# Optimization experiments

Measured on AMD Instinct MI355X. Metric: run time of the kernel, lower is better.

The kernel has to match this reference:

```python
import jax, jax.numpy as jnp
import numpy as np

NUM_LSTMS = 2
INPUT_DIM = 1
HIDDEN_DIM = 32
OUTPUT_DIM = 1


def _init_cell(key, in_dim, hid):
    k1, k2, k3, k4 = jax.random.split(key, 4)
    s = 1.0 / np.sqrt(hid)
    Wih = jax.random.uniform(k1, (4 * hid, in_dim), minval=-s, maxval=s, dtype=jnp.float32)
    Whh = jax.random.uniform(k2, (4 * hid, hid), minval=-s, maxval=s, dtype=jnp.float32)
    bih = jax.random.uniform(k3, (4 * hid,), minval=-s, maxval=s, dtype=jnp.float32)
    bhh = jax.random.uniform(k4, (4 * hid,), minval=-s, maxval=s, dtype=jnp.float32)
    # forget-gate bias (second quarter in PyTorch i,f,g,o layout) filled with 1.0
    bih = bih.at[hid:2 * hid].set(1.0)
    bhh = bhh.at[hid:2 * hid].set(1.0)
    return Wih, Whh, bih, bhh


def setup_inputs() -> dict:
    key = jax.random.key(0)
    kx, k0, k1, kl = jax.random.split(key, 4)
    B, T = 2048, 1024
    x = jax.random.normal(kx, (B, T), dtype=jnp.float32)
    Wih0, Whh0, bih0, bhh0 = _init_cell(k0, INPUT_DIM, HIDDEN_DIM)
    Wih1, Whh1, bih1, bhh1 = _init_cell(k1, HIDDEN_DIM, HIDDEN_DIM)
    kw, kb = jax.random.split(kl)
    s = 1.0 / np.sqrt(HIDDEN_DIM)
    Wlin = jax.random.uniform(kw, (OUTPUT_DIM, HIDDEN_DIM), minval=-s, maxval=s, dtype=jnp.float32)
    blin = jax.random.uniform(kb, (OUTPUT_DIM,), minval=-s, maxval=s, dtype=jnp.float32)
    return {"x": x, "Wih0": Wih0, "Whh0": Whh0, "bih0": bih0, "bhh0": bhh0,
            "Wih1": Wih1, "Whh1": Whh1, "bih1": bih1, "bhh1": bhh1,
            "Wlin": Wlin, "blin": blin}


def _lstm_cell(x_t, h, c, Wih, Whh, bih, bhh):
    # PyTorch LSTMCell gate layout: i, f, g, o
    g = x_t @ Wih.T + bih + h @ Whh.T + bhh  # [B, 4H]
    i, f, gg, o = jnp.split(g, 4, axis=-1)
    i = jax.nn.sigmoid(i)
    f = jax.nn.sigmoid(f)
    gg = jnp.tanh(gg)
    o = jax.nn.sigmoid(o)
    c_new = f * c + i * gg
    h_new = o * jnp.tanh(c_new)
    return h_new, c_new


def reference(x, Wih0, Whh0, bih0, bhh0, Wih1, Whh1, bih1, bhh1, Wlin, blin):
    B, T = x.shape
    params = [(Wih0, Whh0, bih0, bhh0), (Wih1, Whh1, bih1, bhh1)]
    h0 = [jnp.zeros((B, HIDDEN_DIM), jnp.float32) for _ in range(NUM_LSTMS)]
    c0 = [jnp.zeros((B, HIDDEN_DIM), jnp.float32) for _ in range(NUM_LSTMS)]

    xs = x.T[:, :, None]  # [T, B, 1]

    def step(carry, x_t):
        hs, cs = carry
        hs, cs = list(hs), list(cs)
        inp = x_t
        for j in range(NUM_LSTMS):
            hs[j], cs[j] = _lstm_cell(inp, hs[j], cs[j], *params[j])
            inp = hs[j]
        out = hs[-1] @ Wlin.T + blin  # [B, 1]
        return (tuple(hs), tuple(cs)), out

    _, outs = jax.lax.scan(step, (tuple(h0), tuple(c0)), xs)  # [T, B, 1]
    return outs[:, :, 0].T  # [B, T]
```

## Files before the change

kernel.cpp:

```cpp
#include <hip/hip_runtime.h>


typedef _Float16 h2 __attribute__((ext_vector_type(2)));
typedef _Float16 h8 __attribute__((ext_vector_type(8)));

constexpr int BATCH = 2048;
constexpr int TLEN  = 1024;
constexpr int HID   = 32;
constexpr float L2E = 1.44269504088896f;

union H8U { h8 v; h2 p[4]; };

static __device__ __forceinline__ float rcp_f(float v){ return __builtin_amdgcn_rcpf(v); }
static __device__ __forceinline__ float exp2_f(float v){ return __builtin_amdgcn_exp2f(v); }
static __device__ __forceinline__ float bcastf(float v, int k){
    return __int_as_float(__builtin_amdgcn_readlane(__float_as_int(v), k));
}
static __device__ __forceinline__ float dot2(h2 a, h2 b, float c){
    return __builtin_amdgcn_fdot2(a, b, c, false);
}
static __device__ __forceinline__ int pki(float a, float b){
    h2 r; r.x = (_Float16)a; r.y = (_Float16)b;
    return __builtin_bit_cast(int, r);
}
static __device__ __forceinline__ h2 asp(int v){ return __builtin_bit_cast(h2, v); }
static __device__ __forceinline__ float xchg32(float v, int xaddr){
    return __int_as_float(__builtin_amdgcn_ds_bpermute(xaddr, __float_as_int(v)));
}

__global__ void __launch_bounds__(256) __attribute__((amdgpu_waves_per_eu(2, 2)))
lstm2_v9(const float* __restrict__ x,
         const float* __restrict__ Wih0, const float* __restrict__ Whh0,
         const float* __restrict__ bih0, const float* __restrict__ bhh0,
         const float* __restrict__ Wih1, const float* __restrict__ Whh1,
         const float* __restrict__ bih1, const float* __restrict__ bhh1,
         const float* __restrict__ Wlin, const float* __restrict__ blin,
         float* __restrict__ out)
{
    const int tid  = threadIdx.x;
    const int lane = tid & 63;
    const int w    = tid >> 6;
    const int b    = blockIdx.x * 4 + w;
    const int j    = lane & 31;
    const int hi   = lane >> 5;
    const int rowA = hi * 64 + j;
    const int rowB = rowA + 32;
    const int xaddr = (lane ^ 32) << 2;

    __shared__ alignas(16) _Float16 hb0s[4][32];
    __shared__ alignas(16) _Float16 hstore[4][64][40];
    __shared__ alignas(16) _Float16 wls[4][32];

    _Float16* hb0p = &hb0s[w][0];

    wls[w][j] = (_Float16)Wlin[j];

    int wA0i[16], wB0i[16], iA1i[16], iB1i[16], hA1i[16], hB1i[16];
    #pragma unroll
    for (int m = 0; m < 16; ++m){
        wA0i[m] = pki(Whh0[rowA * HID + 2*m], Whh0[rowA * HID + 2*m + 1]);
        wB0i[m] = pki(Whh0[rowB * HID + 2*m], Whh0[rowB * HID + 2*m + 1]);
        iA1i[m] = pki(Wih1[rowA * HID + 2*m], Wih1[rowA * HID + 2*m + 1]);
        iB1i[m] = pki(Wih1[rowB * HID + 2*m], Wih1[rowB * HID + 2*m + 1]);
        hA1i[m] = pki(Whh1[rowA * HID + 2*m], Whh1[rowA * HID + 2*m + 1]);
        hB1i[m] = pki(Whh1[rowB * HID + 2*m], Whh1[rowB * HID + 2*m + 1]);
    }
    #pragma unroll
    for (int m = 0; m < 16; ++m){
        asm volatile("" : "+v"(wA0i[m]), "+v"(wB0i[m]), "+v"(iA1i[m]),
                          "+v"(iB1i[m]), "+v"(hA1i[m]), "+v"(hB1i[m]));
    }

    float wa0 = Wih0[rowA];
    float wb0 = Wih0[rowB];
    float ba0 = bih0[rowA] + bhh0[rowA];
    float bb0 = bih0[rowB] + bhh0[rowB];
    float ba1 = bih1[rowA] + bhh1[rowA];
    float bb1 = bih1[rowB] + bhh1[rowB];
    float bl  = blin[0];
    asm volatile("" : "+v"(wa0), "+v"(wb0), "+v"(ba0), "+v"(bb0),
                      "+v"(ba1), "+v"(bb1), "+v"(bl));

    const float kA = hi ? (-2.0f * L2E) : (-L2E);
    const float mA = hi ?  2.0f : 1.0f;
    const float cA = hi ? -1.0f : 0.0f;

    float c0 = 0.0f, c1 = 0.0f;
    H8U hp0[4], hp1[4];
    #pragma unroll
    for (int m = 0; m < 4; ++m){
        hp0[m].v = (h8)(_Float16)0.0f;
        hp1[m].v = (h8)(_Float16)0.0f;
    }

    const float* xrow = x   + (size_t)b * TLEN;
    float*       orow = out + (size_t)b * TLEN;

    for (int tc = 0; tc < TLEN / 64; ++tc){
        const float xchunk = xrow[tc * 64 + lane];

        for (int tt = 0; tt < 64; ++tt){
            const float xt = bcastf(xchunk, tt);

            float ga  = __builtin_fmaf(wa0, xt, ba0);
            float gb  = __builtin_fmaf(wb0, xt, bb0);
            float ga2 = 0.0f, gb2 = 0.0f;
            #pragma unroll
            for (int m = 0; m < 4; ++m){
                ga  = dot2(asp(wA0i[4*m+0]), hp0[m].p[0], ga );
                gb  = dot2(asp(wB0i[4*m+0]), hp0[m].p[0], gb );
                ga2 = dot2(asp(wA0i[4*m+1]), hp0[m].p[1], ga2);
                gb2 = dot2(asp(wB0i[4*m+1]), hp0[m].p[1], gb2);
                ga  = dot2(asp(wA0i[4*m+2]), hp0[m].p[2], ga );
                gb  = dot2(asp(wB0i[4*m+2]), hp0[m].p[2], gb );
                ga2 = dot2(asp(wA0i[4*m+3]), hp0[m].p[3], ga2);
                gb2 = dot2(asp(wB0i[4*m+3]), hp0[m].p[3], gb2);
            }
            ga += ga2; gb += gb2;

            float act_a = __builtin_fmaf(mA, rcp_f(1.0f + exp2_f(ga * kA)), cA);
            float act_b = rcp_f(1.0f + exp2_f(gb * (-L2E)));
            const float oa = xchg32(act_a, xaddr);
            const float ob = xchg32(act_b, xaddr);
            {
                const float fsel = hi ? ob : act_b;
                const float osel = hi ? act_b : ob;
                c0 = __builtin_fmaf(fsel, c0, act_a * oa);
                const float t0 = __builtin_fmaf(2.0f,
                        rcp_f(1.0f + exp2_f(c0 * (-2.0f * L2E))), -1.0f);
                const float h0 = osel * t0;
                hb0p[j] = (_Float16)h0;
            }
            {
                const h8* hv = (const h8*)hb0p;
                #pragma unroll
                for (int m = 0; m < 4; ++m) hp0[m].v = hv[m];
            }

            float pa = ba1, pb = bb1, pa2 = 0.0f, pb2 = 0.0f;
            float qa = 0.0f, qb = 0.0f, qa2 = 0.0f, qb2 = 0.0f;
            #pragma unroll
            for (int m = 0; m < 4; ++m){
                pa  = dot2(asp(iA1i[4*m+0]), hp0[m].p[0], pa );
                pb  = dot2(asp(iB1i[4*m+0]), hp0[m].p[0], pb );
                qa  = dot2(asp(hA1i[4*m+0]), hp1[m].p[0], qa );
                qb  = dot2(asp(hB1i[4*m+0]), hp1[m].p[0], qb );
                pa2 = dot2(asp(iA1i[4*m+1]), hp0[m].p[1], pa2);
                pb2 = dot2(asp(iB1i[4*m+1]), hp0[m].p[1], pb2);
                qa2 = dot2(asp(hA1i[4*m+1]), hp1[m].p[1], qa2);
                qb2 = dot2(asp(hB1i[4*m+1]), hp1[m].p[1], qb2);
                pa  = dot2(asp(iA1i[4*m+2]), hp0[m].p[2], pa );
                pb  = dot2(asp(iB1i[4*m+2]), hp0[m].p[2], pb );
                qa  = dot2(asp(hA1i[4*m+2]), hp1[m].p[2], qa );
                qb  = dot2(asp(hB1i[4*m+2]), hp1[m].p[2], qb );
                pa2 = dot2(asp(iA1i[4*m+3]), hp0[m].p[3], pa2);
                pb2 = dot2(asp(iB1i[4*m+3]), hp0[m].p[3], pb2);
                qa2 = dot2(asp(hA1i[4*m+3]), hp1[m].p[3], qa2);
                qb2 = dot2(asp(hB1i[4*m+3]), hp1[m].p[3], qb2);
            }
            const float g1a = (pa + pa2) + (qa + qa2);
            const float g1b = (pb + pb2) + (qb + qb2);

            float act_a1 = __builtin_fmaf(mA, rcp_f(1.0f + exp2_f(g1a * kA)), cA);
            float act_b1 = rcp_f(1.0f + exp2_f(g1b * (-L2E)));
            const float oa1 = xchg32(act_a1, xaddr);
            const float ob1 = xchg32(act_b1, xaddr);
            {
                const float fsel = hi ? ob1 : act_b1;
                const float osel = hi ? act_b1 : ob1;
                c1 = __builtin_fmaf(fsel, c1, act_a1 * oa1);
                const float t1 = __builtin_fmaf(2.0f,
                        rcp_f(1.0f + exp2_f(c1 * (-2.0f * L2E))), -1.0f);
                const float h1 = osel * t1;
                hstore[w][tt][j] = (_Float16)h1;
            }
            {
                const h8* hv = (const h8*)&hstore[w][tt][0];
                #pragma unroll
                for (int m = 0; m < 4; ++m) hp1[m].v = hv[m];
            }
        }

        {
            H8U wl4[4], hr[4];
            const h8* wv = (const h8*)&wls[w][0];
            const h8* hv = (const h8*)&hstore[w][lane][0];
            #pragma unroll
            for (int m = 0; m < 4; ++m){ wl4[m].v = wv[m]; hr[m].v = hv[m]; }
            float y = bl, y2 = 0.0f;
            #pragma unroll
            for (int m = 0; m < 4; ++m){
                y  = dot2(wl4[m].p[0], hr[m].p[0], y );
                y2 = dot2(wl4[m].p[1], hr[m].p[1], y2);
                y  = dot2(wl4[m].p[2], hr[m].p[2], y );
                y2 = dot2(wl4[m].p[3], hr[m].p[3], y2);
            }
            orow[tc * 64 + lane] = y + y2;
        }
    }
}

extern "C" void kernel_launch(void* const* d_in, const int* in_sizes, int n_in,
                              void* d_out, int out_size, void* d_ws, size_t ws_size,
                              hipStream_t stream) {
    const float* x    = (const float*)d_in[0];
    const float* Wih0 = (const float*)d_in[1];
    const float* Whh0 = (const float*)d_in[2];
    const float* bih0 = (const float*)d_in[3];
    const float* bhh0 = (const float*)d_in[4];
    const float* Wih1 = (const float*)d_in[5];
    const float* Whh1 = (const float*)d_in[6];
    const float* bih1 = (const float*)d_in[7];
    const float* bhh1 = (const float*)d_in[8];
    const float* Wlin = (const float*)d_in[9];
    const float* blin = (const float*)d_in[10];
    float* outp = (float*)d_out;

    dim3 block(256);
    dim3 grid(BATCH / 4);
    hipLaunchKernelGGL(lstm2_v9, grid, block, 0, stream,
                       x, Wih0, Whh0, bih0, bhh0, Wih1, Whh1, bih1, bhh1,
                       Wlin, blin, outp);
}
```

Before: 713.5 us.

## Split LSTM layers across producer/consumer waves with a double-buffered ring

Each batch row now has two waves: one runs layer 0 and one runs layer 1, lagging by a step. Layer-0 hidden states pass through a two-slot shared-memory ring, with a block-wide barrier every timestep. The goal is to run the two layers' recurrences concurrently, shortening the serial dependency chain per step and halving per-wave weight registers. The cost is a __syncthreads every step across 8 waves and twice the waves per batch row, which could cut occupancy headroom or add barrier stalls.

Measured after the change: 1.043 ms. 46.2% more time.

```diff
diff --git a/kernel.cpp b/kernel.cpp
--- a/kernel.cpp
+++ b/kernel.cpp
@@ -28,79 +28,58 @@
     return __int_as_float(__builtin_amdgcn_ds_bpermute(xaddr, __float_as_int(v)));
 }
 
-__global__ void __launch_bounds__(256) __attribute__((amdgpu_waves_per_eu(2, 2)))
-lstm2_v9(const float* __restrict__ x,
-         const float* __restrict__ Wih0, const float* __restrict__ Whh0,
-         const float* __restrict__ bih0, const float* __restrict__ bhh0,
-         const float* __restrict__ Wih1, const float* __restrict__ Whh1,
-         const float* __restrict__ bih1, const float* __restrict__ bhh1,
-         const float* __restrict__ Wlin, const float* __restrict__ blin,
-         float* __restrict__ out)
+__global__ void __launch_bounds__(512)
+lstm2_v11(const float* __restrict__ x,
+          const float* __restrict__ Wih0, const float* __restrict__ Whh0,
+          const float* __restrict__ bih0, const float* __restrict__ bhh0,
+          const float* __restrict__ Wih1, const float* __restrict__ Whh1,
+          const float* __restrict__ bih1, const float* __restrict__ bhh1,
+          const float* __restrict__ Wlin, const float* __restrict__ blin,
+          float* __restrict__ out)
 {
     const int tid  = threadIdx.x;
     const int lane = tid & 63;
-    const int w    = tid >> 6;
-    const int b    = blockIdx.x * 4 + w;
+    const int wid  = tid >> 6;
+    const int role = wid >> 2;
+    const int rw   = wid & 3;
+    const int b    = blockIdx.x * 4 + rw;
     const int j    = lane & 31;
     const int hi   = lane >> 5;
     const int rowA = hi * 64 + j;
     const int rowB = rowA + 32;
     const int xaddr = (lane ^ 32) << 2;
 
-    __shared__ alignas(16) _Float16 hb0s[4][32];
+    __shared__ alignas(16) _Float16 ring[2][4][32];
     __shared__ alignas(16) _Float16 hstore[4][64][40];
-    __shared__ alignas(16) _Float16 wls[4][32];
-
-    _Float16* hb0p = &hb0s[w][0];
-
-    wls[w][j] = (_Float16)Wlin[j];
-
-    int wA0i[16], wB0i[16], iA1i[16], iB1i[16], hA1i[16], hB1i[16];
-    #pragma unroll
-    for (int m = 0; m < 16; ++m){
-        wA0i[m] = pki(Whh0[rowA * HID + 2*m], Whh0[rowA * HID + 2*m + 1]);
-        wB0i[m] = pki(Whh0[rowB * HID + 2*m], Whh0[rowB * HID + 2*m + 1]);
-        iA1i[m] = pki(Wih1[rowA * HID + 2*m], Wih1[rowA * HID + 2*m + 1]);
-        iB1i[m] = pki(Wih1[rowB * HID + 2*m], Wih1[rowB * HID + 2*m + 1]);
-        hA1i[m] = pki(Whh1[rowA * HID + 2*m], Whh1[rowA * HID + 2*m + 1]);
-        hB1i[m] = pki(Whh1[rowB * HID + 2*m], Whh1[rowB * HID + 2*m + 1]);
-    }
-    #pragma unroll
-    for (int m = 0; m < 16; ++m){
-        asm volatile("" : "+v"(wA0i[m]), "+v"(wB0i[m]), "+v"(iA1i[m]),
-                          "+v"(iB1i[m]), "+v"(hA1i[m]), "+v"(hB1i[m]));
-    }
-
-    float wa0 = Wih0[rowA];
-    float wb0 = Wih0[rowB];
-    float ba0 = bih0[rowA] + bhh0[rowA];
-    float bb0 = bih0[rowB] + bhh0[rowB];
-    float ba1 = bih1[rowA] + bhh1[rowA];
-    float bb1 = bih1[rowB] + bhh1[rowB];
-    float bl  = blin[0];
-    asm volatile("" : "+v"(wa0), "+v"(wb0), "+v"(ba0), "+v"(bb0),
-                      "+v"(ba1), "+v"(bb1), "+v"(bl));
+    __shared__ alignas(16) _Float16 wls[32];
 
     const float kA = hi ? (-2.0f * L2E) : (-L2E);
     const float mA = hi ?  2.0f : 1.0f;
     const float cA = hi ? -1.0f : 0.0f;
 
-    float c0 = 0.0f, c1 = 0.0f;
-    H8U hp0[4], hp1[4];
-    #pragma unroll
-    for (int m = 0; m < 4; ++m){
-        hp0[m].v = (h8)(_Float16)0.0f;
-        hp1[m].v = (h8)(_Float16)0.0f;
-    }
-
-    const float* xrow = x   + (size_t)b * TLEN;
-    float*       orow = out + (size_t)b * TLEN;
-
-    for (int tc = 0; tc < TLEN / 64; ++tc){
-        const float xchunk = xrow[tc * 64 + lane];
-
-        for (int tt = 0; tt < 64; ++tt){
-            const float xt = bcastf(xchunk, tt);
+    if (role == 0) {
+        int wA0i[16], wB0i[16];
+        #pragma unroll
+        for (int m = 0; m < 16; ++m){
+            wA0i[m] = pki(Whh0[rowA * HID + 2*m], Whh0[rowA * HID + 2*m + 1]);
+            wB0i[m] = pki(Whh0[rowB * HID + 2*m], Whh0[rowB * HID + 2*m + 1]);
+        }
+        float wa0 = Wih0[rowA];
+        float wb0 = Wih0[rowB];
+        float ba0 = bih0[rowA] + bhh0[rowA];
+        float bb0 = bih0[rowB] + bhh0[rowB];
+
+        H8U hp0[4];
+        #pragma unroll
+        for (int m = 0; m < 4; ++m) hp0[m].v = (h8)(_Float16)0.0f;
+        float c0 = 0.0f;
+
+        const float* xrow = x + (size_t)b * TLEN;
+        float xchunk = 0.0f;
+
+        for (int t = 0; t < TLEN; ++t){
+            if ((t & 63) == 0) xchunk = xrow[t + lane];
+            const float xt = bcastf(xchunk, t & 63);
 
             float ga  = __builtin_fmaf(wa0, xt, ba0);
             float gb  = __builtin_fmaf(wb0, xt, bb0);
@@ -122,41 +101,69 @@
             float act_b = rcp_f(1.0f + exp2_f(gb * (-L2E)));
             const float oa = xchg32(act_a, xaddr);
             const float ob = xchg32(act_b, xaddr);
+            const float fsel = hi ? ob : act_b;
+            const float osel = hi ? act_b : ob;
+            c0 = __builtin_fmaf(fsel, c0, act_a * oa);
+            const float t0 = __builtin_fmaf(2.0f,
+                    rcp_f(1.0f + exp2_f(c0 * (-2.0f * L2E))), -1.0f);
+            const float h0 = osel * t0;
+
+            ring[t & 1][rw][j] = (_Float16)h0;
             {
-                const float fsel = hi ? ob : act_b;
-                const float osel = hi ? act_b : ob;
-                c0 = __builtin_fmaf(fsel, c0, act_a * oa);
-                const float t0 = __builtin_fmaf(2.0f,
-                        rcp_f(1.0f + exp2_f(c0 * (-2.0f * L2E))), -1.0f);
-                const float h0 = osel * t0;
-                hb0p[j] = (_Float16)h0;
-            }
+                const h8* hv = (const h8*)&ring[t & 1][rw][0];
+                #pragma unroll
+                for (int m = 0; m < 4; ++m) hp0[m].v = hv[m];
+            }
+            __syncthreads();
+        }
+    } else {
+        int iA1i[16], iB1i[16], hA1i[16], hB1i[16];
+        #pragma unroll
+        for (int m = 0; m < 16; ++m){
+            iA1i[m] = pki(Wih1[rowA * HID + 2*m], Wih1[rowA * HID + 2*m + 1]);
+            iB1i[m] = pki(Wih1[rowB * HID + 2*m], Wih1[rowB * HID + 2*m + 1]);
+            hA1i[m] = pki(Whh1[rowA * HID + 2*m], Whh1[rowA * HID + 2*m + 1]);
+            hB1i[m] = pki(Whh1[rowB * HID + 2*m], Whh1[rowB * HID + 2*m + 1]);
+        }
+        float ba1 = bih1[rowA] + bhh1[rowA];
+        float bb1 = bih1[rowB] + bhh1[rowB];
+        const float bl = blin[0];
+        wls[j] = (_Float16)Wlin[j];
+
+        H8U hp1[4];
+        #pragma unroll
+        for (int m = 0; m < 4; ++m) hp1[m].v = (h8)(_Float16)0.0f;
+        float c1 = 0.0f;
+
+        float* orow = out + (size_t)b * TLEN;
+
+        auto l1_step = [&](int s){
+            H8U hp0r[4];
             {
-                const h8* hv = (const h8*)hb0p;
-                #pragma unroll
-                for (int m = 0; m < 4; ++m) hp0[m].v = hv[m];
-            }
-
+                const h8* hv = (const h8*)&ring[s & 1][rw][0];
+                #pragma unroll
+                for (int m = 0; m < 4; ++m) hp0r[m].v = hv[m];
+            }
             float pa = ba1, pb = bb1, pa2 = 0.0f, pb2 = 0.0f;
             float qa = 0.0f, qb = 0.0f, qa2 = 0.0f, qb2 = 0.0f;
             #pragma unroll
             for (int m = 0; m < 4; ++m){
-                pa  = dot2(asp(iA1i[4*m+0]), hp0[m].p[0], pa );
-                pb  = dot2(asp(iB1i[4*m+0]), hp0[m].p[0], pb );
-                qa  = dot2(asp(hA1i[4*m+0]), hp1[m].p[0], qa );
-                qb  = dot2(asp(hB1i[4*m+0]), hp1[m].p[0], qb );
-                pa2 = dot2(asp(iA1i[4*m+1]), hp0[m].p[1], pa2);
-                pb2 = dot2(asp(iB1i[4*m+1]), hp0[m].p[1], pb2);
-                qa2 = dot2(asp(hA1i[4*m+1]), hp1[m].p[1], qa2);
-                qb2 = dot2(asp(hB1i[4*m+1]), hp1[m].p[1], qb2);
-                pa  = dot2(asp(iA1i[4*m+2]), hp0[m].p[2], pa );
-                pb  = dot2(asp(iB1i[4*m+2]), hp0[m].p[2], pb );
-                qa  = dot2(asp(hA1i[4*m+2]), hp1[m].p[2], qa );
-                qb  = dot2(asp(hB1i[4*m+2]), hp1[m].p[2], qb );
-                pa2 = dot2(asp(iA1i[4*m+3]), hp0[m].p[3], pa2);
-                pb2 = dot2(asp(iB1i[4*m+3]), hp0[m].p[3], pb2);
-                qa2 = dot2(asp(hA1i[4*m+3]), hp1[m].p[3], qa2);
-                qb2 = dot2(asp(hB1i[4*m+3]), hp1[m].p[3], qb2);
+                pa  = dot2(asp(iA1i[4*m+0]), hp0r[m].p[0], pa );
+                pb  = dot2(asp(iB1i[4*m+0]), hp0r[m].p[0], pb );
+                qa  = dot2(asp(hA1i[4*m+0]), hp1[m].p[0],  qa );
+                qb  = dot2(asp(hB1i[4*m+0]), hp1[m].p[0],  qb );
+                pa2 = dot2(asp(iA1i[4*m+1]), hp0r[m].p[1], pa2);
+                pb2 = dot2(asp(iB1i[4*m+1]), hp0r[m].p[1], pb2);
+                qa2 = dot2(asp(hA1i[4*m+1]), hp1[m].p[1],  qa2);
+                qb2 = dot2(asp(hB1i[4*m+1]), hp1[m].p[1],  qb2);
+                pa  = dot2(asp(iA1i[4*m+2]), hp0r[m].p[2], pa );
+                pb  = dot2(asp(iB1i[4*m+2]), hp0r[m].p[2], pb );
+                qa  = dot2(asp(hA1i[4*m+2]), hp1[m].p[2],  qa );
+                qb  = dot2(asp(hB1i[4*m+2]), hp1[m].p[2],  qb );
+                pa2 = dot2(asp(iA1i[4*m+3]), hp0r[m].p[3], pa2);
+                pb2 = dot2(asp(iB1i[4*m+3]), hp0r[m].p[3], pb2);
+                qa2 = dot2(asp(hA1i[4*m+3]), hp1[m].p[3],  qa2);
+                qb2 = dot2(asp(hB1i[4*m+3]), hp1[m].p[3],  qb2);
             }
             const float g1a = (pa + pa2) + (qa + qa2);
             const float g1b = (pb + pb2) + (qb + qb2);
@@ -165,38 +172,42 @@
             float act_b1 = rcp_f(1.0f + exp2_f(g1b * (-L2E)));
             const float oa1 = xchg32(act_a1, xaddr);
             const float ob1 = xchg32(act_b1, xaddr);
+            const float fsel = hi ? ob1 : act_b1;
+            const float osel = hi ? act_b1 : ob1;
+            c1 = __builtin_fmaf(fsel, c1, act_a1 * oa1);
+            const float t1 = __builtin_fmaf(2.0f,
+                    rcp_f(1.0f + exp2_f(c1 * (-2.0f * L2E))), -1.0f);
+            const float h1 = osel * t1;
+
+            hstore[rw][s & 63][j] = (_Float16)h1;
             {
-                const float fsel = hi ? ob1 : act_b1;
-                const float osel = hi ? act_b1 : ob1;
-                c1 = __builtin_fmaf(fsel, c1, act_a1 * oa1);
-                const float t1 = __builtin_fmaf(2.0f,
-                        rcp_f(1.0f + exp2_f(c1 * (-2.0f * L2E))), -1.0f);
-                const float h1 = osel * t1;
-                hstore[w][tt][j] = (_Float16)h1;
-            }
-            {
-                const h8* hv = (const h8*)&hstore[w][tt][0];
+                const h8* hv = (const h8*)&hstore[rw][s & 63][0];
                 #pragma unroll
                 for (int m = 0; m < 4; ++m) hp1[m].v = hv[m];
             }
-        }
-
-        {
-            H8U wl4[4], hr[4];
-            const h8* wv = (const h8*)&wls[w][0];
-            const h8* hv = (const h8*)&hstore[w][lane][0];
-            #pragma unroll
-            for (int m = 0; m < 4; ++m){ wl4[m].v = wv[m]; hr[m].v = hv[m]; }
-            float y = bl, y2 = 0.0f;
-            #pragma unroll
-            for (int m = 0; m < 4; ++m){
-                y  = dot2(wl4[m].p[0], hr[m].p[0], y );
-                y2 = dot2(wl4[m].p[1], hr[m].p[1], y2);
-                y  = dot2(wl4[m].p[2], hr[m].p[2], y );
-                y2 = dot2(wl4[m].p[3], hr[m].p[3], y2);
-            }
-            orow[tc * 64 + lane] = y + y2;
-        }
+            if ((s & 63) == 63){
+                H8U wl4[4], hr[4];
+                const h8* wv = (const h8*)&wls[0];
+                const h8* hv = (const h8*)&hstore[rw][lane][0];
+                #pragma unroll
+                for (int m = 0; m < 4; ++m){ wl4[m].v = wv[m]; hr[m].v = hv[m]; }
+                float y = bl, y2 = 0.0f;
+                #pragma unroll
+                for (int m = 0; m < 4; ++m){
+                    y  = dot2(wl4[m].p[0], hr[m].p[0], y );
+                    y2 = dot2(wl4[m].p[1], hr[m].p[1], y2);
+                    y  = dot2(wl4[m].p[2], hr[m].p[2], y );
+                    y2 = dot2(wl4[m].p[3], hr[m].p[3], y2);
+                }
+                orow[(s - 63) + lane] = y + y2;
+            }
+        };
+
+        for (int t = 0; t < TLEN; ++t){
+            if (t > 0) l1_step(t - 1);
+            __syncthreads();
+        }
+        l1_step(TLEN - 1);
     }
 }
 
@@ -216,9 +227,9 @@
     const float* blin = (const float*)d_in[10];
     float* outp = (float*)d_out;
 
-    dim3 block(256);
+    dim3 block(512);
     dim3 grid(BATCH / 4);
-    hipLaunchKernelGGL(lstm2_v9, grid, block, 0, stream,
+    hipLaunchKernelGGL(lstm2_v11, grid, block, 0, stream,
                        x, Wih0, Whh0, bih0, bhh0, Wih1, Whh1, bih1, bhh1,
                        Wlin, blin, outp);
 }
```
